# Performance work log

Hardware: AMD Instinct MI355X
Metric: run time of the kernel (lower is better)

## Reference

```python
import jax, jax.numpy as jnp
import numpy as np

D = 256      # model dim
H = 4        # heads
L = 6        # layers (shared weights)
N = 32768    # neuron dim; per-head hidden = N//H = 8192
VOCAB = 256
B, T = 2, 2048
EPS = 1e-5


def _ln(x):
    # LayerNorm over last dim, no affine (matches nn.LayerNorm(D, elementwise_affine=False))
    m = jnp.mean(x, axis=-1, keepdims=True)
    v = jnp.mean((x - m) ** 2, axis=-1, keepdims=True)
    return (x - m) * jax.lax.rsqrt(v + EPS)


def _rope(x):
    # x: [B, H, T, d]
    d = x.shape[-1]
    t = x.shape[-2]
    inv_freq = 1.0 / (10000.0 ** (jnp.arange(0, d, 2, dtype=jnp.float32) / d))
    freqs = jnp.arange(t, dtype=jnp.float32)[:, None] * inv_freq[None, :]  # [T, d/2]
    emb = jnp.concatenate([freqs, freqs], axis=-1)                          # [T, d]
    x1, x2 = x[..., : d // 2], x[..., d // 2 :]
    x_rot = jnp.concatenate([-x2, x1], axis=-1)
    return x * jnp.cos(emb) + x_rot * jnp.sin(emb)


def _linear_attn(q, k, v):
    # q,k: [B,H,T,n]; v: [B,T,D]. Raw (unnormalized) scores, STRICTLY causal mask
    # (tril with diagonal=-1, i.e. token t attends to s < t only), no softmax.
    qr = _rope(q)
    kr = _rope(k)
    scores = jnp.einsum('bhtn,bhsn->bhts', qr, kr)  # [B,H,T,T]
    t_idx = jnp.arange(q.shape[-2])
    mask = t_idx[:, None] > t_idx[None, :]          # strict lower triangle
    scores = jnp.where(mask, scores, jnp.zeros((), scores.dtype))
    return jnp.einsum('bhts,bsd->bhtd', scores, v)  # [B,H,T,D]


def setup_inputs() -> dict:
    key = jax.random.key(0)
    ks = jax.random.split(key, 6)
    idx = jax.random.randint(ks[0], (B, T), 0, VOCAB, dtype=jnp.int64)
    std = 0.02
    wte = std * jax.random.normal(ks[1], (VOCAB, D), dtype=jnp.float32)
    encoder = std * jax.random.normal(ks[2], (N, D), dtype=jnp.float32)
    decoder_x = std * jax.random.normal(ks[3], (H, D, N // H), dtype=jnp.float32)
    decoder_y = std * jax.random.normal(ks[4], (H, D, N // H), dtype=jnp.float32)
    readout = std * jax.random.normal(ks[5], (D, VOCAB), dtype=jnp.float32)
    return {"idx": idx, "wte": wte, "encoder": encoder,
            "decoder_x": decoder_x, "decoder_y": decoder_y, "readout": readout}


def reference(idx, wte, encoder, decoder_x, decoder_y, readout):
    # Dropout is identity in eval mode.
    v_ast = _ln(wte[idx])  # [B,T,D]
    for _ in range(L):  # weights SHARED across layers
        x = jax.nn.relu(jnp.einsum('btd,hdn->bhtn', v_ast, decoder_x))  # [B,H,T,N/H]
        a_ast = _linear_attn(x, x, v_ast)                               # [B,H,T,D]
        y = jax.nn.relu(jnp.einsum('bhtd,hdn->bhtn', _ln(a_ast), decoder_y)) * x
        y_flat = jnp.transpose(y, (0, 2, 1, 3)).reshape(y.shape[0], y.shape[2], N)  # [B,T,N]
        v_ast = _ln(v_ast + _ln(y_flat @ encoder))
    return v_ast @ readout  # [B,T,VOCAB]
```

## Files before the change

### kernel.cpp

```cpp
#include <hip/hip_runtime.h>
#include <stdint.h>

typedef unsigned short u16;
typedef __bf16 bfv8 __attribute__((ext_vector_type(8)));
typedef float f32x4 __attribute__((ext_vector_type(4)));

#define BM 128
#define BN 128
#define BK 32

__device__ __forceinline__ float b2f(u16 u){ union{float f; unsigned int i;} x; x.i = ((unsigned int)u)<<16; return x.f; }
__device__ __forceinline__ u16 f2b(float f){ union{float f; unsigned int i;} x; x.f = f; unsigned int r = x.i + 0x7fffu + ((x.i>>16)&1u); return (u16)(r>>16); }

__device__ __forceinline__ void load16_lds(const void* g, void* l){
  __builtin_amdgcn_global_load_lds(
      (const __attribute__((address_space(1))) void*)g,
      (__attribute__((address_space(3))) void*)l, 16, 0, 0);
}

__device__ __forceinline__ void swz(int& bx, int& by, int& bz){
  int gx = gridDim.x, gy = gridDim.y;
  int nw = gx*gy*gridDim.z;
  int flat = blockIdx.x + gx*(blockIdx.y + gy*blockIdx.z);
  int q = nw >> 3, r = nw & 7, xcd = flat & 7, i = flat >> 3;
  int wg = (xcd < r ? xcd*(q+1) : r*(q+1) + (xcd-r)*q) + i;
  bx = wg % gx; int t = wg / gx; by = t % gy; bz = t / gy;
}

struct GP {
  const u16* A; const u16* Bt; const u16* A2; const u16* Bt2;
  const u16* ct; const u16* st;
  float* Cf; u16* Cb; u16* Y;
  int bh0, zs, zm;
};

template<int LDA, int LDB, bool PAIRB>
__device__ __forceinline__ void kloop(const u16* A, const u16* Bt, int m0, int n0,
                                      int kbeg, int kend,
                                      u16 (&As)[2][4096], u16 (&Bs)[2][4096],
                                      f32x4 (&acc)[4][4]){
  const int tid = threadIdx.x;
  const int lane = tid & 63;
  const int wid = tid >> 6;
  const int wm = wid >> 1, wn = wid & 1;
  const int srow = tid >> 2, sslot = tid & 3;
  const int nt = (kend - kbeg) / BK;
  if (nt <= 0) return;

  auto stage = [&](int k0, int buf){
    #pragma unroll
    for (int q = 0; q < 2; ++q){
      int row = q*64 + srow;
      int ks = sslot ^ ((row >> 1) & 3);
      load16_lds(A + (long)(m0 + row)*LDA + (k0 + ks*8), &As[buf][q*2048 + wid*512]);
    }
    #pragma unroll
    for (int q = 0; q < 2; ++q){
      int row = q*64 + srow;
      int ks = sslot ^ ((row >> 1) & 3);
      long brow;
      if (PAIRB){ int wnb = row >> 6, sub = (row >> 5) & 1, r5 = row & 31;
                  brow = n0 + wnb*32 + r5 + sub*4096; }
      else brow = n0 + row;
      load16_lds(Bt + brow*(long)LDB + (k0 + ks*8), &Bs[buf][q*2048 + wid*512]);
    }
  };

  stage(kbeg, 0);
  int cur = 0;
  for (int t = 0; t < nt; ++t){
    int tn = (t+1 < nt) ? (t+1) : t;
    stage(kbeg + tn*BK, cur^1);
    asm volatile("s_waitcnt vmcnt(4)" ::: "memory");
    __builtin_amdgcn_s_barrier();
    bfv8 af[4], bf[4];
    const int r16 = lane & 15, s4 = lane >> 4;
    #pragma unroll
    for (int i = 0; i < 4; ++i){
      int ar = wm*64 + i*16 + r16;
      af[i] = *(const bfv8*)(&As[cur][ar*BK + ((s4 ^ ((ar>>1)&3))*8)]);
      int br = wn*64 + i*16 + r16;
      bf[i] = *(const bfv8*)(&Bs[cur][br*BK + ((s4 ^ ((br>>1)&3))*8)]);
    }
    #pragma unroll
    for (int i = 0; i < 4; ++i)
      #pragma unroll
      for (int j = 0; j < 4; ++j)
        acc[i][j] = __builtin_amdgcn_mfma_f32_16x16x32_bf16(af[i], bf[j], acc[i][j], 0,0,0);
    asm volatile("s_waitcnt lgkmcnt(0)" ::: "memory");
    __builtin_amdgcn_s_barrier();
    cur ^= 1;
  }
  asm volatile("s_waitcnt vmcnt(0)" ::: "memory");
  __builtin_amdgcn_s_barrier();
}

#define EPI_SETUP const int lane = threadIdx.x & 63, wid = threadIdx.x >> 6; \
  const int wm = wid >> 1, wn = wid & 1; const int r16 = lane & 15, s4 = lane >> 4;

__global__ __launch_bounds__(256) void g_rope(GP p){
  int bx, by, bz; swz(bx, by, bz);
  const int m0 = by*BM, n0 = bx*64, z = bz;
  const int bh = p.bh0 + z, b = bh >> 2, h = bh & 3;
  __shared__ u16 As[2][4096], Bs[2][4096];
  f32x4 acc[4][4] = {};
  kloop<256,256,true>(p.A + (long)b*524288, p.Bt + (long)h*2097152, m0, n0, 0, 256, As, Bs, acc);
  EPI_SETUP
  #pragma unroll
  for (int i = 0; i < 4; ++i)
    #pragma unroll
    for (int j = 0; j < 2; ++j){
      int cl = n0 + wn*32 + j*16 + r16;
      #pragma unroll
      for (int v = 0; v < 4; ++v){
        int row = m0 + wm*64 + i*16 + s4*4 + v;
        float x1 = fmaxf(acc[i][j][v], 0.f);
        float x2 = fmaxf(acc[i][j+2][v], 0.f);
        float c = b2f(p.ct[(long)row*4096 + cl]);
        float s = b2f(p.st[(long)row*4096 + cl]);
        p.Cb[(long)z*16777216 + (long)row*8192 + cl]        = f2b(x1*c - x2*s);
        p.Cb[(long)z*16777216 + (long)row*8192 + cl + 4096] = f2b(x2*c + x1*s);
      }
    }
}

__global__ __launch_bounds__(256) void g_qk(GP p){
  int bx, by, bz; swz(bx, by, bz);
  const int m0 = by*BM, n0 = bx*BN, z = bz;
  if (n0 >= m0 + BM) return;
  __shared__ u16 As[2][4096], Bs[2][4096];
  f32x4 acc[4][4] = {};
  const u16* A = p.A + (long)z*16777216;
  kloop<8192,8192,false>(A, A, m0, n0, 0, 8192, As, Bs, acc);
  EPI_SETUP
  #pragma unroll
  for (int i = 0; i < 4; ++i)
    #pragma unroll
    for (int j = 0; j < 4; ++j){
      int col = n0 + wn*64 + j*16 + r16;
      #pragma unroll
      for (int v = 0; v < 4; ++v){
        int row = m0 + wm*64 + i*16 + s4*4 + v;
        p.Cb[(long)z*4194304 + (long)row*2048 + col] = f2b(row > col ? acc[i][j][v] : 0.f);
      }
    }
}

__global__ __launch_bounds__(256) void g_pv(GP p){
  int bx, by, bz; swz(bx, by, bz);
  const int m0 = by*BM, n0 = bx*BN;
  const int head = bz >> p.zs, sl = bz & p.zm;
  const int b = (p.bh0 + head) >> 2;
  const int kc = 2048 >> p.zs;
  const int kbeg = sl*kc;
  const int kend = min(min(2048, m0 + BM), kbeg + kc);
  __shared__ u16 As[2][4096], Bs[2][4096];
  f32x4 acc[4][4] = {};
  kloop<2048,2048,false>(p.A + (long)head*4194304, p.Bt + (long)b*524288, m0, n0, kbeg, kend, As, Bs, acc);
  EPI_SETUP
  #pragma unroll
  for (int i = 0; i < 4; ++i)
    #pragma unroll
    for (int j = 0; j < 4; ++j){
      int col = n0 + wn*64 + j*16 + r16;
      #pragma unroll
      for (int v = 0; v < 4; ++v){
        int row = m0 + wm*64 + i*16 + s4*4 + v;
        p.Cf[(long)bz*524288 + (long)row*256 + col] = acc[i][j][v];
      }
    }
}

__global__ __launch_bounds__(256) void g_fuse(GP p){
  int bx, by, bz; swz(bx, by, bz);
  const int m0 = by*BM, n0 = bx*BN, z = bz;
  const int bh = p.bh0 + z, b = bh >> 2, h = bh & 3;
  __shared__ u16 As[2][4096], Bs[2][4096];
  f32x4 acc1[4][4] = {}, acc2[4][4] = {};
  kloop<256,256,false>(p.A  + (long)z*524288, p.Bt  + (long)h*2097152, m0, n0, 0, 256, As, Bs, acc1);
  kloop<256,256,false>(p.A2 + (long)b*524288, p.Bt2 + (long)h*2097152, m0, n0, 0, 256, As, Bs, acc2);
  EPI_SETUP
  #pragma unroll
  for (int i = 0; i < 4; ++i)
    #pragma unroll
    for (int j = 0; j < 4; ++j){
      int col = n0 + wn*64 + j*16 + r16;
      #pragma unroll
      for (int v = 0; v < 4; ++v){
        int row = m0 + wm*64 + i*16 + s4*4 + v;
        p.Y[(long)z*16777216 + (long)row*8192 + col] =
            f2b(fmaxf(acc1[i][j][v], 0.f) * fmaxf(acc2[i][j][v], 0.f));
      }
    }
}

__global__ __launch_bounds__(256) void g_enc(GP p){
  int bx, by, bz; swz(bx, by, bz);
  const int m0 = by*BM, n0 = bx*BN;
  const int head = bz >> p.zs, sp = bz & p.zm;
  const int h = (p.bh0 + head) & 3;
  const int kc = 8192 >> p.zs;
  const int kbeg = sp*kc, kend = kbeg + kc;
  __shared__ u16 As[2][4096], Bs[2][4096];
  f32x4 acc[4][4] = {};
  kloop<8192,32768,false>(p.A + (long)head*16777216, p.Bt + (long)h*8192, m0, n0, kbeg, kend, As, Bs, acc);
  EPI_SETUP
  #pragma unroll
  for (int i = 0; i < 4; ++i)
    #pragma unroll
    for (int j = 0; j < 4; ++j){
      int col = n0 + wn*64 + j*16 + r16;
      #pragma unroll
      for (int v = 0; v < 4; ++v){
        int row = m0 + wm*64 + i*16 + s4*4 + v;
        p.Cf[(long)bz*524288 + (long)row*256 + col] = acc[i][j][v];
      }
    }
}

__global__ __launch_bounds__(256) void g_out(GP p){
  int bx, by, bz; swz(bx, by, bz); (void)bz;
  const int m0 = by*BM, n0 = bx*BN;
  __shared__ u16 As[2][4096], Bs[2][4096];
  f32x4 acc[4][4] = {};
  kloop<256,256,false>(p.A, p.Bt, m0, n0, 0, 256, As, Bs, acc);
  EPI_SETUP
  #pragma unroll
  for (int i = 0; i < 4; ++i)
    #pragma unroll
    for (int j = 0; j < 4; ++j){
      int col = n0 + wn*64 + j*16 + r16;
      #pragma unroll
      for (int v = 0; v < 4; ++v){
        int row = m0 + wm*64 + i*16 + s4*4 + v;
        p.Cf[(long)row*256 + col] = acc[i][j][v];
      }
    }
}


__device__ __forceinline__ float wave_sum(float v){
  #pragma unroll
  for (int o = 32; o > 0; o >>= 1) v += __shfl_down(v, o, 64);
  return v;
}
__device__ __forceinline__ float block_sum(float v, float* sm){
  v = wave_sum(v);
  __syncthreads();
  if ((threadIdx.x & 63) == 0) sm[threadIdx.x >> 6] = v;
  __syncthreads();
  return sm[0] + sm[1] + sm[2] + sm[3];
}

__global__ __launch_bounds__(256) void k_embed(const int* idx, const float* wte,
                                               float* v, u16* vbf, u16* vbt){
  __shared__ float sm[4];
  __shared__ int is64_s;
  int row = blockIdx.x, d = threadIdx.x;
  int oddnz = (d < 64) ? (idx[2*d + 1] != 0) : 0;
  unsigned long long mb = __ballot(oddnz);
  if (threadIdx.x == 0) is64_s = (mb == 0ULL);
  __syncthreads();
  int tok = is64_s ? idx[2*row] : idx[row];
  float x = wte[tok*256 + d];
  float m = block_sum(x, sm) * (1.f/256.f);
  float dd = x - m;
  float var = block_sum(dd*dd, sm) * (1.f/256.f);
  float y = dd * rsqrtf(var + 1e-5f);
  v[(long)row*256 + d] = y;
  vbf[(long)row*256 + d] = f2b(y);
  int b = row >> 11, t = row & 2047;
  vbt[((long)(b*256 + d))*2048 + t] = f2b(y);
}

__global__ __launch_bounds__(256) void k_ln(const float* abuf, u16* out, int pv){
  __shared__ float sm[4];
  int row = blockIdx.x, d = threadIdx.x;
  int head = row >> 11, t = row & 2047;
  float x = 0.f;
  for (int s = 0; s < pv; ++s) x += abuf[((long)(head*pv + s) << 19) + (long)t*256 + d];
  float m = block_sum(x, sm) * (1.f/256.f);
  float dd = x - m;
  float var = block_sum(dd*dd, sm) * (1.f/256.f);
  out[(long)row*256 + d] = f2b(dd * rsqrtf(var + 1e-5f));
}

__global__ __launch_bounds__(256) void k_acc(const float* part, float* t1,
                                             int bh0, int gc, int ps){
  int t = blockIdx.x, d = threadIdx.x;
  long o = (long)t*256 + d;
  float s0 = 0.f, s1 = 0.f;
  for (int z = 0; z < gc; ++z){
    float v = 0.f;
    for (int sp = 0; sp < ps; ++sp) v += part[((long)(z*ps + sp) << 19) + o];
    if (((bh0 + z) >> 2) == 0) s0 += v; else s1 += v;
  }
  #pragma unroll
  for (int b = 0; b < 2; ++b){
    int lo = bh0 > 4*b ? bh0 : 4*b;
    int hi = (bh0 + gc) < (4*b + 4) ? (bh0 + gc) : (4*b + 4);
    if (lo < hi){
      float s = b == 0 ? s0 : s1;
      if (lo == 4*b) t1[((long)b << 19) + o] = s;
      else           t1[((long)b << 19) + o] += s;
    }
  }
}

__global__ __launch_bounds__(256) void k_finish(const float* t1, float* v, u16* vbf, u16* vbt){
  __shared__ float sm[4];
  int row = blockIdx.x; int d = threadIdx.x;
  int b = row >> 11, t = row & 2047;
  float s = t1[(long)row*256 + d];
  float m = block_sum(s, sm) * (1.f/256.f);
  float dd = s - m;
  float var = block_sum(dd*dd, sm) * (1.f/256.f);
  float u = dd * rsqrtf(var + 1e-5f);
  float wv = v[(long)row*256 + d] + u;
  float m2 = block_sum(wv, sm) * (1.f/256.f);
  float d2 = wv - m2;
  float v2 = block_sum(d2*d2, sm) * (1.f/256.f);
  float y = d2 * rsqrtf(v2 + 1e-5f);
  v[(long)row*256 + d] = y;
  vbf[(long)row*256 + d] = f2b(y);
  vbt[((long)(b*256 + d))*2048 + t] = f2b(y);
}

__global__ __launch_bounds__(256) void k_cossin(u16* ct, u16* st){
  int tid = blockIdx.x*256 + threadIdx.x;
  int t = tid >> 12, i = tid & 4095;
  float f = powf(10000.0f, -(float)i * (1.0f/4096.0f));
  float a = (float)t * f;
  float s, c; sincosf(a, &s, &c);
  ct[tid] = f2b(c); st[tid] = f2b(s);
}

__global__ void k_transpose(const float* in, u16* out, int R, int C, long in_z, long out_z){
  __shared__ float tile[32][33];
  const float* I = in + (long)blockIdx.z * in_z;
  u16* O = out + (long)blockIdx.z * out_z;
  int c0 = blockIdx.x*32, r0 = blockIdx.y*32;
  int tx = threadIdx.x, ty = threadIdx.y;
  #pragma unroll
  for (int k = 0; k < 4; ++k){ int r = ty + k*8; tile[r][tx] = I[(long)(r0+r)*C + c0+tx]; }
  __syncthreads();
  #pragma unroll
  for (int k = 0; k < 4; ++k){ int r = ty + k*8; O[(long)(c0+r)*R + r0+tx] = f2b(tile[tx][r]); }
}


extern "C" void kernel_launch(void* const* d_in, const int* in_sizes, int n_in,
                              void* d_out, int out_size, void* d_ws, size_t ws_size,
                              hipStream_t stream){
  const int*   idx = (const int*)d_in[0];
  const float* wte = (const float*)d_in[1];
  const float* enc = (const float*)d_in[2];
  const float* dx  = (const float*)d_in[3];
  const float* dy  = (const float*)d_in[4];
  const float* ro  = (const float*)d_in[5];
  float* out = (float*)d_out;
  (void)in_sizes; (void)n_in; (void)out_size;

  const size_t base_b = 96600064UL;
  struct Cfg { int gc, pvs, pss; };
  const Cfg lad[] = {{8,2,3},{4,2,3},{2,2,3},{2,1,2},{1,2,3},{1,1,2},{1,0,1},{1,0,0}};
  Cfg cfg = lad[7];
  for (int i = 0; i < 8; ++i){
    size_t ch = (size_t)lad[i].gc * (33554432UL + 8388608UL + 1048576UL
               + ((size_t)(1 << lad[i].pvs))*2097152UL
               + ((size_t)(1 << lad[i].pss))*2097152UL);
    if (base_b + ch <= ws_size){ cfg = lad[i]; break; }
  }
  const int gc = cfg.gc, pvs = cfg.pvs, pss = cfg.pss;
  const int pv = 1 << pvs, ps = 1 << pss;

  char* w = (char*)d_ws;
  size_t off = 0;
  auto alloc = [&](size_t b){ size_t r = off; off += (b + 255) & ~(size_t)255; return r; };
  float* v_ast = (float*)(w + alloc(4096UL*256*4));
  u16*   v_bf  = (u16*)  (w + alloc(4096UL*256*2));
  u16*   v_bt  = (u16*)  (w + alloc(2UL*256*2048*2));
  u16*   dxT   = (u16*)  (w + alloc(4UL*8192*256*2));
  u16*   dyT   = (u16*)  (w + alloc(4UL*8192*256*2));
  u16*   encT  = (u16*)  (w + alloc(256UL*32768*2));
  u16*   roT   = (u16*)  (w + alloc(256UL*256*2));
  u16*   ct    = (u16*)  (w + alloc(2048UL*4096*2));
  u16*   st    = (u16*)  (w + alloc(2048UL*4096*2));
  float* t1    = (float*)(w + alloc(2UL*2048*256*4));
  u16*   xbuf  = (u16*)  (w + alloc((size_t)gc*33554432));
  u16*   scb   = (u16*)  (w + alloc((size_t)gc*8388608));
  u16*   lnAb  = (u16*)  (w + alloc((size_t)gc*1048576));
  float* abuf  = (float*)(w + alloc((size_t)gc*pv*2097152UL));
  float* part  = (float*)(w + alloc((size_t)gc*ps*2097152UL));

  dim3 tb(32, 8);
  k_cossin<<<32768, 256, 0, stream>>>(ct, st);
  k_transpose<<<dim3(256, 8, 4),  tb, 0, stream>>>(dx,  dxT,  256,   8192, 256L*8192, 8192L*256);
  k_transpose<<<dim3(256, 8, 4),  tb, 0, stream>>>(dy,  dyT,  256,   8192, 256L*8192, 8192L*256);
  k_transpose<<<dim3(8, 1024, 1), tb, 0, stream>>>(enc, encT, 32768, 256,  0, 0);
  k_transpose<<<dim3(8, 8, 1),    tb, 0, stream>>>(ro,  roT,  256,   256,  0, 0);
  k_embed<<<4096, 256, 0, stream>>>(idx, wte, v_ast, v_bf, v_bt);

  for (int l = 0; l < 6; ++l){
    for (int bh0 = 0; bh0 < 8; bh0 += gc){
      { GP g{}; g.bh0=bh0; g.A=v_bf; g.Bt=dxT; g.ct=ct; g.st=st; g.Cb=xbuf;
        g_rope<<<dim3(64,16,gc), 256, 0, stream>>>(g); }
      { GP g{}; g.bh0=bh0; g.A=xbuf; g.Cb=scb;
        g_qk<<<dim3(16,16,gc), 256, 0, stream>>>(g); }
      { GP g{}; g.bh0=bh0; g.A=scb; g.Bt=v_bt; g.Cf=abuf; g.zs=pvs; g.zm=pv-1;
        g_pv<<<dim3(2,16,gc*pv), 256, 0, stream>>>(g); }
      k_ln<<<gc*2048, 256, 0, stream>>>(abuf, lnAb, pv);
      { GP g{}; g.bh0=bh0; g.A=lnAb; g.Bt=dyT; g.A2=v_bf; g.Bt2=dxT; g.Y=xbuf;
        g_fuse<<<dim3(64,16,gc), 256, 0, stream>>>(g); }
      { GP g{}; g.bh0=bh0; g.A=xbuf; g.Bt=encT; g.Cf=part; g.zs=pss; g.zm=ps-1;
        g_enc<<<dim3(2,16,gc*ps), 256, 0, stream>>>(g); }
      k_acc<<<2048, 256, 0, stream>>>(part, t1, bh0, gc, ps);
    }
    k_finish<<<4096, 256, 0, stream>>>(t1, v_ast, v_bf, v_bt);
  }
  { GP g{}; g.A=v_bf; g.Bt=roT; g.Cf=out;
    g_out<<<dim3(2,32,1), 256, 0, stream>>>(g); }
}
```

Baseline: 7.998 ms.

## Shrink QK^T tiles to 64x64 to skip masked upper-triangle work

Rewrites the causal QK^T score kernel to use 64x64 tiles with a dedicated inline double-buffered MFMA loop instead of the shared 128x128 kloop. Finer tiles let blocks lying fully above the diagonal skip the K=8192 reduction; those within the old 128-tile footprint just write zeros, the rest exit early. The goal is to cut wasted matmul work on the triangular mask. The cost is lower arithmetic intensity and more global reloads per FLOP from the smaller tiles.

```diff
diff --git a/kernel.cpp b/kernel.cpp
--- a/kernel.cpp
+++ b/kernel.cpp
@@ -126,22 +126,64 @@
 
 __global__ __launch_bounds__(256) void g_qk(GP p){
   int bx, by, bz; swz(bx, by, bz);
-  const int m0 = by*BM, n0 = bx*BN, z = bz;
-  if (n0 >= m0 + BM) return;
-  __shared__ u16 As[2][4096], Bs[2][4096];
-  f32x4 acc[4][4] = {};
+  const int m0 = by*64, n0 = bx*64, z = bz;
+  if (n0 >= ((m0 & ~64) + 128)) return;
+  u16* C = p.Cb + (long)z*4194304;
+  if (n0 >= m0 + 64){
+    int r = threadIdx.x >> 2, c0 = (threadIdx.x & 3) * 16;
+    uint4 zz = {0,0,0,0};
+    *(uint4*)(C + (long)(m0+r)*2048 + n0 + c0)     = zz;
+    *(uint4*)(C + (long)(m0+r)*2048 + n0 + c0 + 8) = zz;
+    return;
+  }
   const u16* A = p.A + (long)z*16777216;
-  kloop<8192,8192,false>(A, A, m0, n0, 0, 8192, As, Bs, acc);
-  EPI_SETUP
-  #pragma unroll
-  for (int i = 0; i < 4; ++i)
-    #pragma unroll
-    for (int j = 0; j < 4; ++j){
-      int col = n0 + wn*64 + j*16 + r16;
-      #pragma unroll
-      for (int v = 0; v < 4; ++v){
-        int row = m0 + wm*64 + i*16 + s4*4 + v;
-        p.Cb[(long)z*4194304 + (long)row*2048 + col] = f2b(row > col ? acc[i][j][v] : 0.f);
+  __shared__ u16 As[2][2048], Bs[2][2048];
+  const int tid = threadIdx.x, lane = tid & 63, wid = tid >> 6;
+  const int wm = wid >> 1, wn = wid & 1;
+  f32x4 acc[2][2] = {};
+  const int srow = wid*16 + (lane >> 2);
+  const int sslot = lane & 3;
+  auto stage = [&](int k0, int buf){
+    int ks = sslot ^ ((srow >> 1) & 3);
+    load16_lds(A + (long)(m0 + srow)*8192 + (k0 + ks*8), &As[buf][wid*512]);
+    load16_lds(A + (long)(n0 + srow)*8192 + (k0 + ks*8), &Bs[buf][wid*512]);
+  };
+  stage(0, 0);
+  int cur = 0;
+  for (int t = 0; t < 256; ++t){
+    int tn = (t+1 < 256) ? (t+1) : t;
+    stage(tn*BK, cur^1);
+    asm volatile("s_waitcnt vmcnt(2)" ::: "memory");
+    __builtin_amdgcn_s_barrier();
+    bfv8 af[2], bf[2];
+    const int r16 = lane & 15, s4 = lane >> 4;
+    #pragma unroll
+    for (int i = 0; i < 2; ++i){
+      int ar = wm*32 + i*16 + r16;
+      af[i] = *(const bfv8*)(&As[cur][ar*32 + ((s4 ^ ((ar>>1)&3))*8)]);
+      int br = wn*32 + i*16 + r16;
+      bf[i] = *(const bfv8*)(&Bs[cur][br*32 + ((s4 ^ ((br>>1)&3))*8)]);
+    }
+    #pragma unroll
+    for (int i = 0; i < 2; ++i)
+      #pragma unroll
+      for (int j = 0; j < 2; ++j)
+        acc[i][j] = __builtin_amdgcn_mfma_f32_16x16x32_bf16(af[i], bf[j], acc[i][j], 0,0,0);
+    asm volatile("s_waitcnt lgkmcnt(0)" ::: "memory");
+    __builtin_amdgcn_s_barrier();
+    cur ^= 1;
+  }
+  asm volatile("s_waitcnt vmcnt(0)" ::: "memory");
+  const int r16 = lane & 15, s4 = lane >> 4;
+  #pragma unroll
+  for (int i = 0; i < 2; ++i)
+    #pragma unroll
+    for (int j = 0; j < 2; ++j){
+      int col = n0 + wn*32 + j*16 + r16;
+      #pragma unroll
+      for (int v = 0; v < 4; ++v){
+        int row = m0 + wm*32 + i*16 + s4*4 + v;
+        C[(long)row*2048 + col] = f2b(row > col ? acc[i][j][v] : 0.f);
       }
     }
 }
@@ -406,7 +448,7 @@
       { GP g{}; g.bh0=bh0; g.A=v_bf; g.Bt=dxT; g.ct=ct; g.st=st; g.Cb=xbuf;
         g_rope<<<dim3(64,16,gc), 256, 0, stream>>>(g); }
       { GP g{}; g.bh0=bh0; g.A=xbuf; g.Cb=scb;
-        g_qk<<<dim3(16,16,gc), 256, 0, stream>>>(g); }
+        g_qk<<<dim3(32,32,gc), 256, 0, stream>>>(g); }
       { GP g{}; g.bh0=bh0; g.A=scb; g.Bt=v_bt; g.Cf=abuf; g.zs=pvs; g.zm=pv-1;
         g_pv<<<dim3(2,16,gc*pv), 256, 0, stream>>>(g); }
       k_ln<<<gc*2048, 256, 0, stream>>>(abuf, lnAb, pv);
```

Result: slower. 11.40 ms (+42.5%).

## Split-K the QK score GEMM, move causal masking to a kernel, peel kloop

Applied to the files above, without the earlier changes.

The QK^T score GEMM can now be split in two along its 8192-long K dimension. Each half writes bf16 partial scores to its own buffer, and a new k_scmask kernel adds the halves and applies the strict causal mask. The workspace ladder picks whether to split (qs) alongside the existing group and split sizes. The shared kloop also peels its last iteration, so it no longer issues a redundant stage load on the final tile. The cost is an extra elementwise pass over the score matrix on every configuration, including the top one that does not split, plus two bf16 roundings before the add when the split is used.

```diff
diff --git a/kernel.cpp b/kernel.cpp
--- a/kernel.cpp
+++ b/kernel.cpp
@@ -11,6 +11,8 @@
 
 __device__ __forceinline__ float b2f(u16 u){ union{float f; unsigned int i;} x; x.i = ((unsigned int)u)<<16; return x.f; }
 __device__ __forceinline__ u16 f2b(float f){ union{float f; unsigned int i;} x; x.f = f; unsigned int r = x.i + 0x7fffu + ((x.i>>16)&1u); return (u16)(r>>16); }
+
+union U8 { uint4 v; u16 h[8]; };
 
 __device__ __forceinline__ void load16_lds(const void* g, void* l){
   __builtin_amdgcn_global_load_lds(
@@ -65,33 +67,38 @@
       load16_lds(Bt + brow*(long)LDB + (k0 + ks*8), &Bs[buf][q*2048 + wid*512]);
     }
   };
+  auto compute = [&](int buf){
+    bfv8 af[4], bf[4];
+    const int r16 = lane & 15, s4 = lane >> 4;
+    #pragma unroll
+    for (int i = 0; i < 4; ++i){
+      int ar = wm*64 + i*16 + r16;
+      af[i] = *(const bfv8*)(&As[buf][ar*BK + ((s4 ^ ((ar>>1)&3))*8)]);
+      int br = wn*64 + i*16 + r16;
+      bf[i] = *(const bfv8*)(&Bs[buf][br*BK + ((s4 ^ ((br>>1)&3))*8)]);
+    }
+    #pragma unroll
+    for (int i = 0; i < 4; ++i)
+      #pragma unroll
+      for (int j = 0; j < 4; ++j)
+        acc[i][j] = __builtin_amdgcn_mfma_f32_16x16x32_bf16(af[i], bf[j], acc[i][j], 0,0,0);
+  };
 
   stage(kbeg, 0);
   int cur = 0;
-  for (int t = 0; t < nt; ++t){
-    int tn = (t+1 < nt) ? (t+1) : t;
-    stage(kbeg + tn*BK, cur^1);
+  for (int t = 0; t < nt-1; ++t){
+    stage(kbeg + (t+1)*BK, cur^1);
     asm volatile("s_waitcnt vmcnt(4)" ::: "memory");
     __builtin_amdgcn_s_barrier();
-    bfv8 af[4], bf[4];
-    const int r16 = lane & 15, s4 = lane >> 4;
-    #pragma unroll
-    for (int i = 0; i < 4; ++i){
-      int ar = wm*64 + i*16 + r16;
-      af[i] = *(const bfv8*)(&As[cur][ar*BK + ((s4 ^ ((ar>>1)&3))*8)]);
-      int br = wn*64 + i*16 + r16;
-      bf[i] = *(const bfv8*)(&Bs[cur][br*BK + ((s4 ^ ((br>>1)&3))*8)]);
-    }
-    #pragma unroll
-    for (int i = 0; i < 4; ++i)
-      #pragma unroll
-      for (int j = 0; j < 4; ++j)
-        acc[i][j] = __builtin_amdgcn_mfma_f32_16x16x32_bf16(af[i], bf[j], acc[i][j], 0,0,0);
+    compute(cur);
     asm volatile("s_waitcnt lgkmcnt(0)" ::: "memory");
     __builtin_amdgcn_s_barrier();
     cur ^= 1;
   }
   asm volatile("s_waitcnt vmcnt(0)" ::: "memory");
+  __builtin_amdgcn_s_barrier();
+  compute(cur);
+  asm volatile("s_waitcnt lgkmcnt(0)" ::: "memory");
   __builtin_amdgcn_s_barrier();
 }
 
@@ -126,12 +133,16 @@
 
 __global__ __launch_bounds__(256) void g_qk(GP p){
   int bx, by, bz; swz(bx, by, bz);
-  const int m0 = by*BM, n0 = bx*BN, z = bz;
+  const int m0 = by*BM, n0 = bx*BN;
   if (n0 >= m0 + BM) return;
+  const int head = bz >> p.zs, split = bz & p.zm;
+  const int kc = 8192 >> p.zs;
+  const int kbeg = split*kc, kend = kbeg + kc;
+  const u16* A = p.A + (long)head*16777216;
   __shared__ u16 As[2][4096], Bs[2][4096];
   f32x4 acc[4][4] = {};
-  const u16* A = p.A + (long)z*16777216;
-  kloop<8192,8192,false>(A, A, m0, n0, 0, 8192, As, Bs, acc);
+  kloop<8192,8192,false>(A, A, m0, n0, kbeg, kend, As, Bs, acc);
+  u16* C = (split == 0 ? p.Cb : p.Y) + (long)head*4194304;
   EPI_SETUP
   #pragma unroll
   for (int i = 0; i < 4; ++i)
@@ -141,9 +152,27 @@
       #pragma unroll
       for (int v = 0; v < 4; ++v){
         int row = m0 + wm*64 + i*16 + s4*4 + v;
-        p.Cb[(long)z*4194304 + (long)row*2048 + col] = f2b(row > col ? acc[i][j][v] : 0.f);
-      }
-    }
+        C[(long)row*2048 + col] = f2b(acc[i][j][v]);
+      }
+    }
+}
+
+__global__ __launch_bounds__(256) void k_scmask(const u16* pq1, u16* scb, int qs){
+  int t = blockIdx.x, z = blockIdx.y;
+  u16* S = scb + (long)z*4194304 + (long)t*2048;
+  const u16* P = pq1 + (long)z*4194304 + (long)t*2048;
+  int slen = (t & ~127) + 128;
+  for (int c = threadIdx.x*8; c < slen; c += 2048){
+    U8 a, b, o;
+    a.v = *(const uint4*)(S + c);
+    if (qs == 2) b.v = *(const uint4*)(P + c);
+    #pragma unroll
+    for (int j = 0; j < 8; ++j){
+      float s = b2f(a.h[j]) + (qs == 2 ? b2f(b.h[j]) : 0.f);
+      o.h[j] = f2b((t > c + j) ? s : 0.f);
+    }
+    *(uint4*)(S + c) = o.v;
+  }
 }
 
 __global__ __launch_bounds__(256) void g_pv(GP p){
@@ -362,17 +391,20 @@
   (void)in_sizes; (void)n_in; (void)out_size;
 
   const size_t base_b = 96600064UL;
-  struct Cfg { int gc, pvs, pss; };
-  const Cfg lad[] = {{8,2,3},{4,2,3},{2,2,3},{2,1,2},{1,2,3},{1,1,2},{1,0,1},{1,0,0}};
+  struct Cfg { int gc, pvs, pss, qs; };
+  const Cfg lad[] = {{8,2,3,1},{4,2,3,2},{2,2,3,2},{2,2,3,1},
+                     {1,2,3,2},{1,1,2,2},{1,1,2,1},{1,0,0,1}};
   Cfg cfg = lad[7];
   for (int i = 0; i < 8; ++i){
-    size_t ch = (size_t)lad[i].gc * (33554432UL + 8388608UL + 1048576UL
+    size_t ch = (size_t)lad[i].gc * (33554432UL + 8388608UL
+               + (lad[i].qs == 2 ? 8388608UL : 0UL) + 1048576UL
                + ((size_t)(1 << lad[i].pvs))*2097152UL
                + ((size_t)(1 << lad[i].pss))*2097152UL);
     if (base_b + ch <= ws_size){ cfg = lad[i]; break; }
   }
-  const int gc = cfg.gc, pvs = cfg.pvs, pss = cfg.pss;
+  const int gc = cfg.gc, pvs = cfg.pvs, pss = cfg.pss, qs = cfg.qs;
   const int pv = 1 << pvs, ps = 1 << pss;
+  const int qzs = (qs == 2) ? 1 : 0, qzm = qs - 1;
 
   char* w = (char*)d_ws;
   size_t off = 0;
@@ -389,9 +421,11 @@
   float* t1    = (float*)(w + alloc(2UL*2048*256*4));
   u16*   xbuf  = (u16*)  (w + alloc((size_t)gc*33554432));
   u16*   scb   = (u16*)  (w + alloc((size_t)gc*8388608));
+  u16*   pq1   = (u16*)  (w + alloc(qs == 2 ? (size_t)gc*8388608 : 0));
   u16*   lnAb  = (u16*)  (w + alloc((size_t)gc*1048576));
   float* abuf  = (float*)(w + alloc((size_t)gc*pv*2097152UL));
   float* part  = (float*)(w + alloc((size_t)gc*ps*2097152UL));
+  if (qs != 2) pq1 = scb;
 
   dim3 tb(32, 8);
   k_cossin<<<32768, 256, 0, stream>>>(ct, st);
@@ -405,8 +439,9 @@
     for (int bh0 = 0; bh0 < 8; bh0 += gc){
       { GP g{}; g.bh0=bh0; g.A=v_bf; g.Bt=dxT; g.ct=ct; g.st=st; g.Cb=xbuf;
         g_rope<<<dim3(64,16,gc), 256, 0, stream>>>(g); }
-      { GP g{}; g.bh0=bh0; g.A=xbuf; g.Cb=scb;
-        g_qk<<<dim3(16,16,gc), 256, 0, stream>>>(g); }
+      { GP g{}; g.bh0=bh0; g.A=xbuf; g.Cb=scb; g.Y=pq1; g.zs=qzs; g.zm=qzm;
+        g_qk<<<dim3(16,16,gc*qs), 256, 0, stream>>>(g); }
+      k_scmask<<<dim3(2048, gc), 256, 0, stream>>>(pq1, scb, qs);
       { GP g{}; g.bh0=bh0; g.A=scb; g.Bt=v_bt; g.Cf=abuf; g.zs=pvs; g.zm=pv-1;
         g_pv<<<dim3(2,16,gc*pv), 256, 0, stream>>>(g); }
       k_ln<<<gc*2048, 256, 0, stream>>>(abuf, lnAb, pv);
```

Result: slower. 9.355 ms (+17.0%).

## Give QK kernel a dedicated BK=64 triple-buffered pipeline and drop redundant tail load

Applied to the files above, without the earlier changes.

The shared kloop now peels its last iteration, so it no longer issues a redundant duplicate stage load on the final step. The g_qk kernel (K=8192, the largest reduction) gets its own loop with BK=64 tiles, triple-buffered LDS and two-tile lookahead, using an 8-way XOR swizzle. The goal is to hide more global-memory latency and halve the barrier count per K. In exchange it uses 96KB of LDS per block, which can cut occupancy.

```diff
diff --git a/kernel.cpp b/kernel.cpp
--- a/kernel.cpp
+++ b/kernel.cpp
@@ -65,33 +65,38 @@
       load16_lds(Bt + brow*(long)LDB + (k0 + ks*8), &Bs[buf][q*2048 + wid*512]);
     }
   };
+  auto compute = [&](int buf){
+    bfv8 af[4], bf[4];
+    const int r16 = lane & 15, s4 = lane >> 4;
+    #pragma unroll
+    for (int i = 0; i < 4; ++i){
+      int ar = wm*64 + i*16 + r16;
+      af[i] = *(const bfv8*)(&As[buf][ar*BK + ((s4 ^ ((ar>>1)&3))*8)]);
+      int br = wn*64 + i*16 + r16;
+      bf[i] = *(const bfv8*)(&Bs[buf][br*BK + ((s4 ^ ((br>>1)&3))*8)]);
+    }
+    #pragma unroll
+    for (int i = 0; i < 4; ++i)
+      #pragma unroll
+      for (int j = 0; j < 4; ++j)
+        acc[i][j] = __builtin_amdgcn_mfma_f32_16x16x32_bf16(af[i], bf[j], acc[i][j], 0,0,0);
+  };
 
   stage(kbeg, 0);
   int cur = 0;
-  for (int t = 0; t < nt; ++t){
-    int tn = (t+1 < nt) ? (t+1) : t;
-    stage(kbeg + tn*BK, cur^1);
+  for (int t = 0; t < nt-1; ++t){
+    stage(kbeg + (t+1)*BK, cur^1);
     asm volatile("s_waitcnt vmcnt(4)" ::: "memory");
     __builtin_amdgcn_s_barrier();
-    bfv8 af[4], bf[4];
-    const int r16 = lane & 15, s4 = lane >> 4;
-    #pragma unroll
-    for (int i = 0; i < 4; ++i){
-      int ar = wm*64 + i*16 + r16;
-      af[i] = *(const bfv8*)(&As[cur][ar*BK + ((s4 ^ ((ar>>1)&3))*8)]);
-      int br = wn*64 + i*16 + r16;
-      bf[i] = *(const bfv8*)(&Bs[cur][br*BK + ((s4 ^ ((br>>1)&3))*8)]);
-    }
-    #pragma unroll
-    for (int i = 0; i < 4; ++i)
-      #pragma unroll
-      for (int j = 0; j < 4; ++j)
-        acc[i][j] = __builtin_amdgcn_mfma_f32_16x16x32_bf16(af[i], bf[j], acc[i][j], 0,0,0);
+    compute(cur);
     asm volatile("s_waitcnt lgkmcnt(0)" ::: "memory");
     __builtin_amdgcn_s_barrier();
     cur ^= 1;
   }
   asm volatile("s_waitcnt vmcnt(0)" ::: "memory");
+  __builtin_amdgcn_s_barrier();
+  compute(cur);
+  asm volatile("s_waitcnt lgkmcnt(0)" ::: "memory");
   __builtin_amdgcn_s_barrier();
 }
 
@@ -128,11 +133,69 @@
   int bx, by, bz; swz(bx, by, bz);
   const int m0 = by*BM, n0 = bx*BN, z = bz;
   if (n0 >= m0 + BM) return;
-  __shared__ u16 As[2][4096], Bs[2][4096];
+  const u16* A = p.A + (long)z*16777216;
+  __shared__ u16 As[3][8192], Bs[3][8192];
+  const int tid = threadIdx.x, lane = tid & 63, wid = tid >> 6;
+  const int wm = wid >> 1, wn = wid & 1;
+  const int rr = tid >> 3, slot = tid & 7;
   f32x4 acc[4][4] = {};
-  const u16* A = p.A + (long)z*16777216;
-  kloop<8192,8192,false>(A, A, m0, n0, 0, 8192, As, Bs, acc);
-  EPI_SETUP
+
+  auto stage = [&](int k0, int buf){
+    #pragma unroll
+    for (int q = 0; q < 4; ++q){
+      int row = q*32 + rr;
+      int ks = slot ^ (row & 7);
+      load16_lds(A + (long)(m0 + row)*8192 + (k0 + ks*8), &As[buf][q*2048 + rr*64 + slot*8]);
+    }
+    #pragma unroll
+    for (int q = 0; q < 4; ++q){
+      int row = q*32 + rr;
+      int ks = slot ^ (row & 7);
+      load16_lds(A + (long)(n0 + row)*8192 + (k0 + ks*8), &Bs[buf][q*2048 + rr*64 + slot*8]);
+    }
+  };
+  auto compute = [&](int buf){
+    const int r16 = lane & 15, s4 = lane >> 4;
+    #pragma unroll
+    for (int kk = 0; kk < 2; ++kk){
+      bfv8 af[4], bf[4];
+      #pragma unroll
+      for (int i = 0; i < 4; ++i){
+        int ar = wm*64 + i*16 + r16;
+        af[i] = *(const bfv8*)(&As[buf][ar*64 + (((kk*4 + s4) ^ (ar & 7))*8)]);
+        int br = wn*64 + i*16 + r16;
+        bf[i] = *(const bfv8*)(&Bs[buf][br*64 + (((kk*4 + s4) ^ (br & 7))*8)]);
+      }
+      #pragma unroll
+      for (int i = 0; i < 4; ++i)
+        #pragma unroll
+        for (int j = 0; j < 4; ++j)
+          acc[i][j] = __builtin_amdgcn_mfma_f32_16x16x32_bf16(af[i], bf[j], acc[i][j], 0,0,0);
+    }
+  };
+
+  const int nt = 128;
+  stage(0, 0);
+  stage(64, 1);
+  for (int t = 0; t < nt-2; ++t){
+    stage((t+2)*64, (t+2)%3);
+    asm volatile("s_waitcnt vmcnt(16)" ::: "memory");
+    __builtin_amdgcn_s_barrier();
+    compute(t%3);
+    asm volatile("s_waitcnt lgkmcnt(0)" ::: "memory");
+    __builtin_amdgcn_s_barrier();
+  }
+  asm volatile("s_waitcnt vmcnt(8)" ::: "memory");
+  __builtin_amdgcn_s_barrier();
+  compute((nt-2)%3);
+  asm volatile("s_waitcnt lgkmcnt(0)" ::: "memory");
+  __builtin_amdgcn_s_barrier();
+  asm volatile("s_waitcnt vmcnt(0)" ::: "memory");
+  __builtin_amdgcn_s_barrier();
+  compute((nt-1)%3);
+
+  u16* C = p.Cb + (long)z*4194304;
+  const int r16 = lane & 15, s4 = lane >> 4;
   #pragma unroll
   for (int i = 0; i < 4; ++i)
     #pragma unroll
@@ -141,7 +204,7 @@
       #pragma unroll
       for (int v = 0; v < 4; ++v){
         int row = m0 + wm*64 + i*16 + s4*4 + v;
-        p.Cb[(long)z*4194304 + (long)row*2048 + col] = f2b(row > col ? acc[i][j][v] : 0.f);
+        C[(long)row*2048 + col] = f2b(row > col ? acc[i][j][v] : 0.f);
       }
     }
 }
```

Result: slower. 10.92 ms (+36.5%).
